# Optimization experiments

Measured on AMD Instinct MI355X. Metric: run time of the kernel, lower is better.

The kernel has to match this reference:

```python
import jax, jax.numpy as jnp
import numpy as np

S, D, H, MLP = 2048, 1024, 16, 4096
DK = D // H
EPS = 1e-5  # torch LayerNorm default


def setup_inputs() -> dict:
    key = jax.random.key(0)
    ks = jax.random.split(key, 8)
    init = lambda k, shape, fan_in: jax.random.normal(k, shape, jnp.float32) * (fan_in ** -0.5)
    return {
        "x": jax.random.normal(ks[0], (S, D), jnp.float32),
        "wq": init(ks[1], (D, D), D), "bq": jnp.zeros((D,), jnp.float32),
        "wk": init(ks[2], (D, D), D), "bk": jnp.zeros((D,), jnp.float32),
        "wv": init(ks[3], (D, D), D), "bv": jnp.zeros((D,), jnp.float32),
        "wo": init(ks[4], (D, D), D), "bo": jnp.zeros((D,), jnp.float32),
        "w1": init(ks[5], (D, MLP), D), "b1": jnp.zeros((MLP,), jnp.float32),
        "w2": init(ks[6], (MLP, D), MLP), "b2": jnp.zeros((D,), jnp.float32),
        "ln1_g": jnp.ones((D,), jnp.float32), "ln1_b": jnp.zeros((D,), jnp.float32),
        "ln2_g": jnp.ones((D,), jnp.float32), "ln2_b": jnp.zeros((D,), jnp.float32),
    }


def _layernorm(x, g, b):
    m = jnp.mean(x, axis=-1, keepdims=True)
    v = jnp.var(x, axis=-1, keepdims=True)
    return (x - m) * jax.lax.rsqrt(v + EPS) * g + b


def reference(x, wq, bq, wk, bk, wv, bv, wo, bo, w1, b1, w2, b2, ln1_g, ln1_b, ln2_g, ln2_b):
    # --- residual 1: pre-LN multi-head self-attention ---
    h = _layernorm(x, ln1_g, ln1_b)
    q = (h @ wq + bq).reshape(S, H, DK).transpose(1, 0, 2)  # [H,S,DK]
    k = (h @ wk + bk).reshape(S, H, DK).transpose(1, 0, 2)
    v = (h @ wv + bv).reshape(S, H, DK).transpose(1, 0, 2)
    scores = jnp.einsum('hqd,hkd->hqk', q, k) / jnp.sqrt(jnp.float32(DK))  # [H,S,S]
    attn = jax.nn.softmax(scores, axis=-1)
    o = jnp.einsum('hqk,hkd->hqd', attn, v)  # [H,S,DK]
    # Faithful to original: x.contiguous().view(S, -1) is a raw reshape of the
    # [H,S,DK] buffer (no transpose back to [S,H,DK]).
    o = o.reshape(S, D)
    x = x + (o @ wo + bo)
    # --- residual 2: pre-LN GELU FFN ---
    h2 = _layernorm(x, ln2_g, ln2_b)
    f = jax.nn.gelu(h2 @ w1 + b1, approximate=False)  # torch nn.GELU = exact erf
    x = x + (f @ w2 + b2)
    return x
```

## Files before the change

kernel.cpp:

```cpp
#include <hip/hip_runtime.h>


constexpr int kS = 2048, kD = 1024, kH = 16, kDK = 64, kMLP = 4096;
constexpr float kEps = 1e-5f;

using u16 = unsigned short;
using u32 = unsigned int;
typedef float f32x4 __attribute__((ext_vector_type(4)));
typedef short bf16x8 __attribute__((ext_vector_type(8)));

__device__ __forceinline__ u16 f2b(float f) {
  u32 u = __builtin_bit_cast(u32, f);
  return (u16)((u + 0x7fffu + ((u >> 16) & 1u)) >> 16);
}

typedef const __attribute__((address_space(1))) u32* gas1;
typedef __attribute__((address_space(3))) u32* las3;
__device__ __forceinline__ void async16(const void* g, void* l) {
  __builtin_amdgcn_global_load_lds((gas1)g, (las3)l, 16, 0, 0);
}

__global__ __launch_bounds__(256)
void ln_kernel(const float* __restrict__ x, const float* __restrict__ g,
               const float* __restrict__ b, u16* __restrict__ out) {
  __shared__ float red[8];
  const int row = blockIdx.x, tid = threadIdx.x;
  const float4 v = *(const float4*)(x + (size_t)row * kD + tid * 4);
  float s = v.x + v.y + v.z + v.w;
  float ss = v.x * v.x + v.y * v.y + v.z * v.z + v.w * v.w;
#pragma unroll
  for (int d = 1; d < 64; d <<= 1) { s += __shfl_xor(s, d); ss += __shfl_xor(ss, d); }
  if ((tid & 63) == 0) { red[tid >> 6] = s; red[4 + (tid >> 6)] = ss; }
  __syncthreads();
  const float m = (red[0] + red[1] + red[2] + red[3]) * (1.f / kD);
  const float var = (red[4] + red[5] + red[6] + red[7]) * (1.f / kD) - m * m;
  const float r = rsqrtf(var + kEps);
  const float4 gv = *(const float4*)(g + tid * 4);
  const float4 bv = *(const float4*)(b + tid * 4);
  ushort4 o;
  o.x = f2b((v.x - m) * r * gv.x + bv.x);
  o.y = f2b((v.y - m) * r * gv.y + bv.y);
  o.z = f2b((v.z - m) * r * gv.z + bv.z);
  o.w = f2b((v.w - m) * r * gv.w + bv.w);
  *(ushort4*)(out + (size_t)row * kD + tid * 4) = o;
}

__global__ __launch_bounds__(256)
void transpose_cvt(const float* __restrict__ in, u16* __restrict__ out, int R, int C) {
  __shared__ float tile[32][33];
  const int c0 = blockIdx.x * 32, r0 = blockIdx.y * 32;
  const int x = threadIdx.x, y = threadIdx.y;
#pragma unroll
  for (int i = 0; i < 4; ++i)
    tile[y + i * 8][x] = in[(size_t)(r0 + y + i * 8) * C + c0 + x];
  __syncthreads();
#pragma unroll
  for (int i = 0; i < 4; ++i)
    out[(size_t)(c0 + y + i * 8) * R + r0 + x] = f2b(tile[x][y + i * 8]);
}

__global__ void concat_bias(const float* __restrict__ bq, const float* __restrict__ bk,
                            const float* __restrict__ bv, float* __restrict__ out) {
  int i = blockIdx.x * 256 + threadIdx.x;
  out[i] = i < kD ? bq[i] : (i < 2 * kD ? bk[i - kD] : bv[i - 2 * kD]);
}

__global__ __launch_bounds__(256)
void vtrans(const u16* __restrict__ qkv, u16* __restrict__ vt) {
  __shared__ u16 t[64][72];
  const int s0 = blockIdx.x * 64, h = blockIdx.y, tid = threadIdx.x;
#pragma unroll
  for (int r = 0; r < 2; ++r) {
    int chunk = r * 256 + tid, row = chunk >> 3, col = (chunk & 7) * 8;
    uint4 v = *(const uint4*)(qkv + (size_t)(s0 + row) * 3072 + 2 * kD + h * 64 + col);
    *(uint4*)(&t[row][col]) = v;
  }
  __syncthreads();
#pragma unroll
  for (int r = 0; r < 2; ++r) {
    int chunk = r * 256 + tid, drow = chunk >> 3, scol = (chunk & 7) * 8;
    u16 tmp[8];
#pragma unroll
    for (int j = 0; j < 8; ++j) tmp[j] = t[scol + j][drow];
    *(uint4*)(vt + (size_t)h * 64 * kS + (size_t)drow * kS + s0 + scol) = *(uint4*)tmp;
  }
}

template <int EPI>
__global__ __launch_bounds__(512, 1)
void gemm_bt(const u16* __restrict__ A, const u16* __restrict__ Bt,
             const float* __restrict__ bias, void* __restrict__ Cout,
             int N, int K, int Ksub) {
  constexpr int BM = 128, BN = 256, BK = 64;
  __shared__ u16 As[3][BM * BK];
  __shared__ u16 Bs[3][BN * BK];
  const int tid = threadIdx.x;
  const int w = tid >> 6, l = tid & 63;
  const int wm = w >> 2, wn = w & 3;
  const int ln = l & 15, q = l >> 4;
  const int row0 = blockIdx.y * BM, col0 = blockIdx.x * BN;
  const int koff = blockIdx.z * Ksub;
  const int nIter = Ksub / BK;

  const int rS = tid >> 3;
  const int cS = ((tid & 7) ^ (rS & 7)) * 8;
  const u16* Ab0 = A + (size_t)(row0 + rS) * K + koff + cS;
  const u16* Bb0 = Bt + (size_t)(col0 + rS) * K + koff + cS;
  const int dW = w * 512;

  f32x4 acc[4][4] = {};

  auto stage = [&](int t, int b) {
    const int kt = t * BK;
    async16(Ab0 + kt, &As[b][dW]);
    async16(Ab0 + (size_t)64 * K + kt, &As[b][4096 + dW]);
    async16(Bb0 + kt, &Bs[b][dW]);
    async16(Bb0 + (size_t)64 * K + kt, &Bs[b][4096 + dW]);
    async16(Bb0 + (size_t)128 * K + kt, &Bs[b][8192 + dW]);
    async16(Bb0 + (size_t)192 * K + kt, &Bs[b][12288 + dW]);
  };

  stage(0, 0);
  stage(1, 1);
  asm volatile("s_waitcnt vmcnt(6)" ::: "memory");
  __builtin_amdgcn_s_barrier();
  __builtin_amdgcn_sched_barrier(0);

  int bR = 0, bW = 2;
  for (int t = 0; t < nIter; ++t) {
    if (t + 2 < nIter) stage(t + 2, bW);
    const u16* Ar = As[bR];
    const u16* Br = Bs[bR];
#pragma unroll
    for (int ks = 0; ks < 2; ++ks) {
      const int ch = ((ks * 4 + q) ^ (ln & 7)) * 8;
      bf16x8 af[4], bf[4];
#pragma unroll
      for (int i = 0; i < 4; ++i)
        af[i] = *(const bf16x8*)(Ar + (wm * 64 + i * 16 + ln) * 64 + ch);
#pragma unroll
      for (int j = 0; j < 4; ++j)
        bf[j] = *(const bf16x8*)(Br + (wn * 64 + j * 16 + ln) * 64 + ch);
      __builtin_amdgcn_s_setprio(1);
#pragma unroll
      for (int i = 0; i < 4; ++i)
#pragma unroll
        for (int j = 0; j < 4; ++j)
          acc[i][j] = __builtin_amdgcn_mfma_f32_16x16x32_bf16(af[i], bf[j], acc[i][j], 0, 0, 0);
      __builtin_amdgcn_s_setprio(0);
    }
    if (t + 2 < nIter) asm volatile("s_waitcnt vmcnt(6)" ::: "memory");
    else               asm volatile("s_waitcnt vmcnt(0)" ::: "memory");
    __builtin_amdgcn_s_barrier();
    __builtin_amdgcn_sched_barrier(0);
    bR = bR == 2 ? 0 : bR + 1;
    bW = bW == 2 ? 0 : bW + 1;
  }

  float* Pf = nullptr;
  if constexpr (EPI == 3)
    Pf = (float*)Cout + (size_t)blockIdx.z * gridDim.y * BM * N;
#pragma unroll
  for (int i = 0; i < 4; ++i) {
    const int row = row0 + wm * 64 + i * 16 + q * 4;
#pragma unroll
    for (int j = 0; j < 4; ++j) {
      const int col = col0 + wn * 64 + j * 16 + ln;
      float bb = 0.f;
      if constexpr (EPI != 3) bb = bias[col];
#pragma unroll
      for (int r = 0; r < 4; ++r) {
        const size_t idx = (size_t)(row + r) * N + col;
        float v = acc[i][j][r] + bb;
        if constexpr (EPI == 0) {
          ((u16*)Cout)[idx] = f2b(v);
        } else if constexpr (EPI == 1) {
          ((u16*)Cout)[idx] = f2b(0.5f * v * (1.f + erff(v * 0.7071067811865475f)));
        } else {
          Pf[idx] = v;
        }
      }
    }
  }
}

template <int KS>
__global__ __launch_bounds__(256)
void reduce_add(const float* __restrict__ parts, const float* __restrict__ bias,
                const float* __restrict__ res, float* __restrict__ out,
                int N, size_t strideMN) {
  const size_t b = ((size_t)blockIdx.x * 256 + threadIdx.x) * 4;
  float4 a = *(const float4*)(res + b);
  const float4 bv = *(const float4*)(bias + (b & (size_t)(N - 1)));
  a.x += bv.x; a.y += bv.y; a.z += bv.z; a.w += bv.w;
#pragma unroll
  for (int s = 0; s < KS; ++s) {
    const float4 p = *(const float4*)(parts + s * strideMN + b);
    a.x += p.x; a.y += p.y; a.z += p.z; a.w += p.w;
  }
  *(float4*)(out + b) = a;
}

__global__ __launch_bounds__(256, 2)
void flash_attn(const u16* __restrict__ qkv, const u16* __restrict__ vt,
                u16* __restrict__ og) {
  constexpr int LQ = 72;
  constexpr int LV = 136;
  __shared__ u16 Qs[64 * LQ];
  __shared__ u16 Ks[128 * LQ];
  __shared__ u16 Vs[64 * LV];
  __shared__ u16 Ps[4][16 * LV];
  const int tid = threadIdx.x, w = tid >> 6, l = tid & 63;
  const int h = blockIdx.y, q0 = blockIdx.x * 64;

#pragma unroll
  for (int r = 0; r < 2; ++r) {
    int chunk = r * 256 + tid, row = chunk >> 3, col = (chunk & 7) * 8;
    uint4 v = *(const uint4*)(qkv + (size_t)(q0 + row) * 3072 + h * 64 + col);
    *(uint4*)(&Qs[row * LQ + col]) = v;
  }
  __syncthreads();
  bf16x8 qa[2];
#pragma unroll
  for (int kq = 0; kq < 2; ++kq)
    qa[kq] = *(const bf16x8*)(&Qs[(w * 16 + (l & 15)) * LQ + kq * 32 + (l >> 4) * 8]);

  f32x4 oacc[4] = {};
  float mi[4], li[4];
#pragma unroll
  for (int r = 0; r < 4; ++r) { mi[r] = -1e30f; li[r] = 0.f; }

  for (int kt = 0; kt < kS; kt += 128) {
    __syncthreads();
#pragma unroll
    for (int r = 0; r < 4; ++r) {
      int chunk = r * 256 + tid, row = chunk >> 3, col = (chunk & 7) * 8;
      uint4 v = *(const uint4*)(qkv + (size_t)(kt + row) * 3072 + kD + h * 64 + col);
      *(uint4*)(&Ks[row * LQ + col]) = v;
    }
#pragma unroll
    for (int r = 0; r < 4; ++r) {
      int chunk = r * 256 + tid, row = chunk >> 4, col = (chunk & 15) * 8;
      uint4 v = *(const uint4*)(vt + (size_t)h * 64 * kS + (size_t)row * kS + kt + col);
      *(uint4*)(&Vs[row * LV + col]) = v;
    }
    __syncthreads();

    f32x4 s[8];
#pragma unroll
    for (int n = 0; n < 8; ++n) {
      f32x4 z = {};
      bf16x8 kb0 = *(const bf16x8*)(&Ks[(n * 16 + (l & 15)) * LQ + (l >> 4) * 8]);
      bf16x8 kb1 = *(const bf16x8*)(&Ks[(n * 16 + (l & 15)) * LQ + 32 + (l >> 4) * 8]);
      z = __builtin_amdgcn_mfma_f32_16x16x32_bf16(qa[0], kb0, z, 0, 0, 0);
      z = __builtin_amdgcn_mfma_f32_16x16x32_bf16(qa[1], kb1, z, 0, 0, 0);
      s[n] = z;
    }
    float alpha[4];
#pragma unroll
    for (int r = 0; r < 4; ++r) {
      float m = -1e30f;
#pragma unroll
      for (int n = 0; n < 8; ++n) m = fmaxf(m, s[n][r]);
#pragma unroll
      for (int d = 1; d < 16; d <<= 1) m = fmaxf(m, __shfl_xor(m, d));
      m *= 0.125f;
      float mn = fmaxf(mi[r], m);
      alpha[r] = __expf(mi[r] - mn);
      mi[r] = mn;
      li[r] *= alpha[r];
    }
#pragma unroll
    for (int n = 0; n < 4; ++n)
#pragma unroll
      for (int r = 0; r < 4; ++r) oacc[n][r] *= alpha[r];
    float rs[4] = {0.f, 0.f, 0.f, 0.f};
#pragma unroll
    for (int n = 0; n < 8; ++n)
#pragma unroll
      for (int r = 0; r < 4; ++r) {
        float pv = __expf(s[n][r] * 0.125f - mi[r]);
        rs[r] += pv;
        Ps[w][((l >> 4) * 4 + r) * LV + n * 16 + (l & 15)] = f2b(pv);
      }
#pragma unroll
    for (int r = 0; r < 4; ++r) {
      float t = rs[r];
#pragma unroll
      for (int d = 1; d < 16; d <<= 1) t += __shfl_xor(t, d);
      li[r] += t;
    }
    bf16x8 pa[4];
#pragma unroll
    for (int ks = 0; ks < 4; ++ks)
      pa[ks] = *(const bf16x8*)(&Ps[w][(l & 15) * LV + ks * 32 + (l >> 4) * 8]);
#pragma unroll
    for (int n = 0; n < 4; ++n)
#pragma unroll
      for (int ks = 0; ks < 4; ++ks) {
        bf16x8 vb = *(const bf16x8*)(&Vs[(n * 16 + (l & 15)) * LV + ks * 32 + (l >> 4) * 8]);
        oacc[n] = __builtin_amdgcn_mfma_f32_16x16x32_bf16(pa[ks], vb, oacc[n], 0, 0, 0);
      }
  }
#pragma unroll
  for (int r = 0; r < 4; ++r) {
    float inv = 1.f / li[r];
    int srow = q0 + w * 16 + (l >> 4) * 4 + r;
#pragma unroll
    for (int n = 0; n < 4; ++n) {
      int d = n * 16 + (l & 15);
      og[(size_t)h * kS * kDK + (size_t)srow * kDK + d] = f2b(oacc[n][r] * inv);
    }
  }
}

extern "C" void kernel_launch(void* const* d_in, const int* in_sizes, int n_in,
                              void* d_out, int out_size, void* d_ws, size_t ws_size,
                              hipStream_t stream) {
  const float* x = (const float*)d_in[0];
  const float* wq = (const float*)d_in[1];
  const float* bq = (const float*)d_in[2];
  const float* wk = (const float*)d_in[3];
  const float* bk = (const float*)d_in[4];
  const float* wv = (const float*)d_in[5];
  const float* bv = (const float*)d_in[6];
  const float* wo = (const float*)d_in[7];
  const float* bo = (const float*)d_in[8];
  const float* w1 = (const float*)d_in[9];
  const float* b1 = (const float*)d_in[10];
  const float* w2 = (const float*)d_in[11];
  const float* b2 = (const float*)d_in[12];
  const float* ln1g = (const float*)d_in[13];
  const float* ln1b = (const float*)d_in[14];
  const float* ln2g = (const float*)d_in[15];
  const float* ln2b = (const float*)d_in[16];
  float* out = (float*)d_out;

  char* p = (char*)d_ws;
  auto alloc = [&](size_t bytes) { void* q = (void*)p; p += (bytes + 255) & ~(size_t)255; return q; };
  u16* h1 = (u16*)alloc((size_t)kS * kD * 2);
  u16* wqkvt = (u16*)alloc((size_t)3 * kD * kD * 2);
  u16* qkv = (u16*)alloc((size_t)kS * 3 * kD * 2);
  u16* vt = (u16*)alloc((size_t)kH * kDK * kS * 2);
  u16* og = (u16*)alloc((size_t)kS * kD * 2);
  u16* wot = (u16*)alloc((size_t)kD * kD * 2);
  u16* h2 = (u16*)alloc((size_t)kS * kD * 2);
  u16* w1t = (u16*)alloc((size_t)kD * kMLP * 2);
  float* bqkv = (float*)alloc((size_t)3 * kD * 4);
  float* x2 = (float*)alloc((size_t)kS * kD * 4);
  u16* fbuf = (u16*)alloc((size_t)kS * kMLP * 2);
  u16* w2t = (u16*)alloc((size_t)kMLP * kD * 2);
  float* part = (float*)d_ws;
  const size_t strideMN = (size_t)kS * kD;

  dim3 tb(32, 8);
  transpose_cvt<<<dim3(kD / 32, kD / 32), tb, 0, stream>>>(wq, wqkvt, kD, kD);
  transpose_cvt<<<dim3(kD / 32, kD / 32), tb, 0, stream>>>(wk, wqkvt + kD * kD, kD, kD);
  transpose_cvt<<<dim3(kD / 32, kD / 32), tb, 0, stream>>>(wv, wqkvt + 2 * kD * kD, kD, kD);
  transpose_cvt<<<dim3(kD / 32, kD / 32), tb, 0, stream>>>(wo, wot, kD, kD);
  transpose_cvt<<<dim3(kMLP / 32, kD / 32), tb, 0, stream>>>(w1, w1t, kD, kMLP);
  transpose_cvt<<<dim3(kD / 32, kMLP / 32), tb, 0, stream>>>(w2, w2t, kMLP, kD);
  concat_bias<<<dim3(12), dim3(256), 0, stream>>>(bq, bk, bv, bqkv);

  ln_kernel<<<dim3(kS), dim3(256), 0, stream>>>(x, ln1g, ln1b, h1);
  gemm_bt<0><<<dim3(3 * kD / 256, kS / 128, 1), dim3(512), 0, stream>>>(
      h1, wqkvt, bqkv, qkv, 3 * kD, kD, kD);
  vtrans<<<dim3(kS / 64, kH), dim3(256), 0, stream>>>(qkv, vt);
  flash_attn<<<dim3(kS / 64, kH), dim3(256), 0, stream>>>(qkv, vt, og);
  gemm_bt<3><<<dim3(kD / 256, kS / 128, 2), dim3(512), 0, stream>>>(
      og, wot, nullptr, part, kD, kD, kD / 2);
  reduce_add<2><<<dim3(kS * kD / 4 / 256), dim3(256), 0, stream>>>(
      part, bo, x, x2, kD, strideMN);
  ln_kernel<<<dim3(kS), dim3(256), 0, stream>>>(x2, ln2g, ln2b, h2);
  gemm_bt<1><<<dim3(kMLP / 256, kS / 128, 1), dim3(512), 0, stream>>>(
      h2, w1t, b1, fbuf, kMLP, kD, kD);
  gemm_bt<3><<<dim3(kD / 256, kS / 128, 4), dim3(512), 0, stream>>>(
      fbuf, w2t, nullptr, part, kD, kMLP, kMLP / 4);
  reduce_add<4><<<dim3(kS * kD / 4 / 256), dim3(256), 0, stream>>>(
      part, b2, x2, out, kD, strideMN);
}
```

Before: 320.1 us.

## Merge prep kernels, fuse residual reduce with LN2, prefetch K/V in attention

Merges the six weight transpose-convert launches and the bias concat into a single prep kernel that dispatches on block index. Fuses the split-K reduce-add of the output projection with the second LayerNorm, so x2 is not re-read. Flash attention moves to 128-query blocks of 512 threads and prefetches the next K/V tile into registers while the current tile is computed. Together these cut launch overhead and global traffic, at the cost of more registers and LDS per attention block, which lowers occupancy.

```diff
diff --git a/kernel.cpp b/kernel.cpp
--- a/kernel.cpp
+++ b/kernel.cpp
@@ -46,10 +46,33 @@
 }
 
 __global__ __launch_bounds__(256)
-void transpose_cvt(const float* __restrict__ in, u16* __restrict__ out, int R, int C) {
+void prep(const float* __restrict__ wq, const float* __restrict__ wk,
+          const float* __restrict__ wv, const float* __restrict__ wo,
+          const float* __restrict__ w1, const float* __restrict__ w2,
+          const float* __restrict__ bq, const float* __restrict__ bk,
+          const float* __restrict__ bv, u16* __restrict__ wqkvt,
+          u16* __restrict__ wot, u16* __restrict__ w1t, u16* __restrict__ w2t,
+          float* __restrict__ bqkv) {
+  const int bid = blockIdx.x;
+  const int x = threadIdx.x, y = threadIdx.y;
+  if (bid >= 12288) {
+    int i = (bid - 12288) * 256 + y * 32 + x;
+    bqkv[i] = i < kD ? bq[i] : (i < 2 * kD ? bk[i - kD] : bv[i - 2 * kD]);
+    return;
+  }
+  const float* in; u16* out; int R, C, t;
+  if (bid < 4096) {
+    int j = bid >> 10; t = bid & 1023; R = kD; C = kD;
+    in = j == 0 ? wq : j == 1 ? wk : j == 2 ? wv : wo;
+    out = j == 3 ? wot : wqkvt + (size_t)j * kD * kD;
+  } else if (bid < 8192) {
+    t = bid - 4096; R = kD; C = kMLP; in = w1; out = w1t;
+  } else {
+    t = bid - 8192; R = kMLP; C = kD; in = w2; out = w2t;
+  }
+  const int nbx = C >> 5;
+  const int c0 = (t % nbx) * 32, r0 = (t / nbx) * 32;
   __shared__ float tile[32][33];
-  const int c0 = blockIdx.x * 32, r0 = blockIdx.y * 32;
-  const int x = threadIdx.x, y = threadIdx.y;
 #pragma unroll
   for (int i = 0; i < 4; ++i)
     tile[y + i * 8][x] = in[(size_t)(r0 + y + i * 8) * C + c0 + x];
@@ -57,12 +80,6 @@
 #pragma unroll
   for (int i = 0; i < 4; ++i)
     out[(size_t)(c0 + y + i * 8) * R + r0 + x] = f2b(tile[x][y + i * 8]);
-}
-
-__global__ void concat_bias(const float* __restrict__ bq, const float* __restrict__ bk,
-                            const float* __restrict__ bv, float* __restrict__ out) {
-  int i = blockIdx.x * 256 + threadIdx.x;
-  out[i] = i < kD ? bq[i] : (i < 2 * kD ? bk[i - kD] : bv[i - 2 * kD]);
 }
 
 __global__ __launch_bounds__(256)
@@ -201,24 +218,69 @@
   *(float4*)(out + b) = a;
 }
 
-__global__ __launch_bounds__(256, 2)
+template <int KS>
+__global__ __launch_bounds__(256)
+void reduce_ln(const float* __restrict__ parts, const float* __restrict__ bias,
+               const float* __restrict__ res, const float* __restrict__ g,
+               const float* __restrict__ b, float* __restrict__ x2out,
+               u16* __restrict__ h2out, size_t strideMN) {
+  __shared__ float red[8];
+  const int row = blockIdx.x, tid = threadIdx.x;
+  const size_t base = (size_t)row * kD + tid * 4;
+  float4 a = *(const float4*)(res + base);
+  const float4 bv = *(const float4*)(bias + tid * 4);
+  a.x += bv.x; a.y += bv.y; a.z += bv.z; a.w += bv.w;
+#pragma unroll
+  for (int s = 0; s < KS; ++s) {
+    const float4 p = *(const float4*)(parts + s * strideMN + base);
+    a.x += p.x; a.y += p.y; a.z += p.z; a.w += p.w;
+  }
+  *(float4*)(x2out + base) = a;
+  float s1 = a.x + a.y + a.z + a.w;
+  float ss = a.x * a.x + a.y * a.y + a.z * a.z + a.w * a.w;
+#pragma unroll
+  for (int d = 1; d < 64; d <<= 1) { s1 += __shfl_xor(s1, d); ss += __shfl_xor(ss, d); }
+  if ((tid & 63) == 0) { red[tid >> 6] = s1; red[4 + (tid >> 6)] = ss; }
+  __syncthreads();
+  const float m = (red[0] + red[1] + red[2] + red[3]) * (1.f / kD);
+  const float var = (red[4] + red[5] + red[6] + red[7]) * (1.f / kD) - m * m;
+  const float rr = rsqrtf(var + kEps);
+  const float4 gv = *(const float4*)(g + tid * 4);
+  const float4 bbv = *(const float4*)(b + tid * 4);
+  ushort4 o;
+  o.x = f2b((a.x - m) * rr * gv.x + bbv.x);
+  o.y = f2b((a.y - m) * rr * gv.y + bbv.y);
+  o.z = f2b((a.z - m) * rr * gv.z + bbv.z);
+  o.w = f2b((a.w - m) * rr * gv.w + bbv.w);
+  *(ushort4*)(h2out + base) = o;
+}
+
+__global__ __launch_bounds__(512, 1)
 void flash_attn(const u16* __restrict__ qkv, const u16* __restrict__ vt,
                 u16* __restrict__ og) {
   constexpr int LQ = 72;
   constexpr int LV = 136;
-  __shared__ u16 Qs[64 * LQ];
+  __shared__ u16 Qs[128 * LQ];
   __shared__ u16 Ks[128 * LQ];
   __shared__ u16 Vs[64 * LV];
-  __shared__ u16 Ps[4][16 * LV];
+  __shared__ u16 Ps[8][16 * LV];
   const int tid = threadIdx.x, w = tid >> 6, l = tid & 63;
-  const int h = blockIdx.y, q0 = blockIdx.x * 64;
+  const int h = blockIdx.y, q0 = blockIdx.x * 128;
 
 #pragma unroll
   for (int r = 0; r < 2; ++r) {
-    int chunk = r * 256 + tid, row = chunk >> 3, col = (chunk & 7) * 8;
+    int chunk = r * 512 + tid, row = chunk >> 3, col = (chunk & 7) * 8;
     uint4 v = *(const uint4*)(qkv + (size_t)(q0 + row) * 3072 + h * 64 + col);
     *(uint4*)(&Qs[row * LQ + col]) = v;
   }
+  const int krA = tid >> 3, kcA = (tid & 7) * 8;
+  const int vrA = tid >> 4, vcA = (tid & 15) * 8;
+  uint4 kreg[2], vreg[2];
+#pragma unroll
+  for (int r = 0; r < 2; ++r) {
+    kreg[r] = *(const uint4*)(qkv + (size_t)(r * 64 + krA) * 3072 + kD + h * 64 + kcA);
+    vreg[r] = *(const uint4*)(vt + (size_t)h * 64 * kS + (size_t)(r * 32 + vrA) * kS + vcA);
+  }
   __syncthreads();
   bf16x8 qa[2];
 #pragma unroll
@@ -231,20 +293,19 @@
   for (int r = 0; r < 4; ++r) { mi[r] = -1e30f; li[r] = 0.f; }
 
   for (int kt = 0; kt < kS; kt += 128) {
+#pragma unroll
+    for (int r = 0; r < 2; ++r) {
+      *(uint4*)(&Ks[(r * 64 + krA) * LQ + kcA]) = kreg[r];
+      *(uint4*)(&Vs[(r * 32 + vrA) * LV + vcA]) = vreg[r];
+    }
     __syncthreads();
-#pragma unroll
-    for (int r = 0; r < 4; ++r) {
-      int chunk = r * 256 + tid, row = chunk >> 3, col = (chunk & 7) * 8;
-      uint4 v = *(const uint4*)(qkv + (size_t)(kt + row) * 3072 + kD + h * 64 + col);
-      *(uint4*)(&Ks[row * LQ + col]) = v;
-    }
-#pragma unroll
-    for (int r = 0; r < 4; ++r) {
-      int chunk = r * 256 + tid, row = chunk >> 4, col = (chunk & 15) * 8;
-      uint4 v = *(const uint4*)(vt + (size_t)h * 64 * kS + (size_t)row * kS + kt + col);
-      *(uint4*)(&Vs[row * LV + col]) = v;
-    }
-    __syncthreads();
+    if (kt + 128 < kS) {
+#pragma unroll
+      for (int r = 0; r < 2; ++r) {
+        kreg[r] = *(const uint4*)(qkv + (size_t)(kt + 128 + r * 64 + krA) * 3072 + kD + h * 64 + kcA);
+        vreg[r] = *(const uint4*)(vt + (size_t)h * 64 * kS + (size_t)(r * 32 + vrA) * kS + kt + 128 + vcA);
+      }
+    }
 
     f32x4 s[8];
 #pragma unroll
@@ -301,6 +362,7 @@
         bf16x8 vb = *(const bf16x8*)(&Vs[(n * 16 + (l & 15)) * LV + ks * 32 + (l >> 4) * 8]);
         oacc[n] = __builtin_amdgcn_mfma_f32_16x16x32_bf16(pa[ks], vb, oacc[n], 0, 0, 0);
       }
+    __syncthreads();
   }
 #pragma unroll
   for (int r = 0; r < 4; ++r) {
@@ -353,25 +415,18 @@
   float* part = (float*)d_ws;
   const size_t strideMN = (size_t)kS * kD;
 
-  dim3 tb(32, 8);
-  transpose_cvt<<<dim3(kD / 32, kD / 32), tb, 0, stream>>>(wq, wqkvt, kD, kD);
-  transpose_cvt<<<dim3(kD / 32, kD / 32), tb, 0, stream>>>(wk, wqkvt + kD * kD, kD, kD);
-  transpose_cvt<<<dim3(kD / 32, kD / 32), tb, 0, stream>>>(wv, wqkvt + 2 * kD * kD, kD, kD);
-  transpose_cvt<<<dim3(kD / 32, kD / 32), tb, 0, stream>>>(wo, wot, kD, kD);
-  transpose_cvt<<<dim3(kMLP / 32, kD / 32), tb, 0, stream>>>(w1, w1t, kD, kMLP);
-  transpose_cvt<<<dim3(kD / 32, kMLP / 32), tb, 0, stream>>>(w2, w2t, kMLP, kD);
-  concat_bias<<<dim3(12), dim3(256), 0, stream>>>(bq, bk, bv, bqkv);
+  prep<<<dim3(12300), dim3(32, 8), 0, stream>>>(
+      wq, wk, wv, wo, w1, w2, bq, bk, bv, wqkvt, wot, w1t, w2t, bqkv);
 
   ln_kernel<<<dim3(kS), dim3(256), 0, stream>>>(x, ln1g, ln1b, h1);
   gemm_bt<0><<<dim3(3 * kD / 256, kS / 128, 1), dim3(512), 0, stream>>>(
       h1, wqkvt, bqkv, qkv, 3 * kD, kD, kD);
   vtrans<<<dim3(kS / 64, kH), dim3(256), 0, stream>>>(qkv, vt);
-  flash_attn<<<dim3(kS / 64, kH), dim3(256), 0, stream>>>(qkv, vt, og);
+  flash_attn<<<dim3(kS / 128, kH), dim3(512), 0, stream>>>(qkv, vt, og);
   gemm_bt<3><<<dim3(kD / 256, kS / 128, 2), dim3(512), 0, stream>>>(
       og, wot, nullptr, part, kD, kD, kD / 2);
-  reduce_add<2><<<dim3(kS * kD / 4 / 256), dim3(256), 0, stream>>>(
-      part, bo, x, x2, kD, strideMN);
-  ln_kernel<<<dim3(kS), dim3(256), 0, stream>>>(x2, ln2g, ln2b, h2);
+  reduce_ln<2><<<dim3(kS), dim3(256), 0, stream>>>(
+      part, bo, x, ln2g, ln2b, x2, h2, strideMN);
   gemm_bt<1><<<dim3(kMLP / 256, kS / 128, 1), dim3(512), 0, stream>>>(
       h2, w1t, b1, fbuf, kMLP, kD, kD);
   gemm_bt<3><<<dim3(kD / 256, kS / 128, 4), dim3(512), 0, stream>>>(
```

Measured after the change: 326.2 us. No clear change (+1.9%).
